# Kernel tuning notes

Measured on AMD Instinct MI355X. Metric: run time of the kernel, lower is better.

The kernel has to match this reference:

```python
import jax, jax.numpy as jnp
import numpy as np

N_ENTITIES = 100000
N_EDGES = 1250000
N_RELATIONS = 32
D = 64


def setup_inputs() -> dict:
    key = jax.random.key(0)
    k1, k2, k3, k4 = jax.random.split(key, 4)
    entity_emb = jax.random.normal(k1, (N_ENTITIES, D), dtype=jnp.float32)
    edge_index = jax.random.randint(k2, (2, N_EDGES), 0, N_ENTITIES, dtype=jnp.int64)
    edge_type = jax.random.randint(k3, (N_EDGES,), 0, N_RELATIONS, dtype=jnp.int64)
    weight = jax.random.normal(k4, (N_RELATIONS, D), dtype=jnp.float32)
    return {"entity_emb": entity_emb, "edge_index": edge_index,
            "edge_type": edge_type, "weight": weight}


def reference(entity_emb, edge_index, edge_type, weight):
    n_entities = entity_emb.shape[0]
    head, tail = edge_index[0], edge_index[1]
    # gather tail entity embeddings and relation embeddings, elementwise multiply
    neigh_relation_emb = entity_emb[tail] * weight[edge_type]  # [E, D]
    # scatter_mean by head index
    sums = jax.ops.segment_sum(neigh_relation_emb, head, num_segments=n_entities)
    counts = jax.ops.segment_sum(jnp.ones((head.shape[0],), dtype=entity_emb.dtype),
                                 head, num_segments=n_entities)
    entity_agg = sums / jnp.maximum(counts, 1.0)[:, None]  # empty segments -> 0
    return entity_agg
```

## Files before the change

### kernel.cpp

```cpp
#include <hip/hip_runtime.h>

#define D 64
#define BIN_SHIFT 7
#define BIN_SIZE 128
#define MAX_BINS 1024
#define BINCAP 2560
#define K1_THREADS 512
#define K1_EPT 10
#define K1_EPB (K1_THREADS * K1_EPT)
#define K2_THREADS 512
#define NREL 32


__device__ __forceinline__ float bf2f(unsigned short u) {
    union { unsigned i; float f; } x; x.i = ((unsigned)u) << 16; return x.f;
}

__global__ void cvt_kernel(const float* __restrict__ emb,
                           unsigned short* __restrict__ emb16,
                           int* __restrict__ binCount, int nbins, long n4) {
    long i = (long)blockIdx.x * blockDim.x + threadIdx.x;
    if (i < (long)nbins) binCount[i] = 0;
    if (i >= n4) return;
    float4 v = ((const float4*)emb)[i];
    ushort4 o;
    unsigned b;
    b = __float_as_uint(v.x); o.x = (unsigned short)((b + 0x7FFF + ((b >> 16) & 1)) >> 16);
    b = __float_as_uint(v.y); o.y = (unsigned short)((b + 0x7FFF + ((b >> 16) & 1)) >> 16);
    b = __float_as_uint(v.z); o.z = (unsigned short)((b + 0x7FFF + ((b >> 16) & 1)) >> 16);
    b = __float_as_uint(v.w); o.w = (unsigned short)((b + 0x7FFF + ((b >> 16) & 1)) >> 16);
    ((ushort4*)emb16)[i] = o;
}

__global__ void __launch_bounds__(K1_THREADS)
bin_sort_kernel(const int* __restrict__ head,
                const int* __restrict__ tail,
                const int* __restrict__ etype,
                int* __restrict__ binCount,
                unsigned* __restrict__ recs,
                int nbins, int n_edges) {
    __shared__ unsigned srec[K1_EPB];
    __shared__ int hist[MAX_BINS];
    __shared__ int base[MAX_BINS + 1];
    __shared__ int cur[MAX_BINS];
    __shared__ int gpos[MAX_BINS];
    __shared__ unsigned short binof[K1_EPB];
    __shared__ int wtot[8];
    __shared__ int wexcl[8];

    int tid = threadIdx.x;
    for (int b = tid; b < MAX_BINS; b += K1_THREADS) hist[b] = 0;
    __syncthreads();

    long blockBase = (long)blockIdx.x * K1_EPB;
    int nvalid = (int)(((long)n_edges - blockBase < (long)K1_EPB)
                       ? ((long)n_edges - blockBase) : (long)K1_EPB);

    unsigned rv[K1_EPT]; int bv[K1_EPT];
#pragma unroll
    for (int k = 0; k < K1_EPT; k++) {
        long e = blockBase + (long)k * K1_THREADS + tid;
        if (e < n_edges) {
            int h = head[e];
            bv[k] = h >> BIN_SHIFT;
            rv[k] = (unsigned)tail[e] | ((unsigned)etype[e] << 17)
                  | ((unsigned)(h & (BIN_SIZE - 1)) << 22);
            atomicAdd(&hist[bv[k]], 1);
        } else bv[k] = -1;
    }
    __syncthreads();

    int s0 = hist[2 * tid], s1 = hist[2 * tid + 1];
    int v = s0 + s1;
    int lane = tid & 63, wv = tid >> 6;
#pragma unroll
    for (int s = 1; s < 64; s <<= 1) {
        int x = __shfl_up(v, s);
        if (lane >= s) v += x;
    }
    if (lane == 63) wtot[wv] = v;
    __syncthreads();
    if (tid < 8) {
        int t = wtot[tid];
        int a = t;
#pragma unroll
        for (int s = 1; s < 8; s <<= 1) {
            int x = __shfl_up(a, s);
            if (tid >= s) a += x;
        }
        wexcl[tid] = a - t;
    }
    __syncthreads();
    int incl = v + wexcl[wv];
    int pairExcl = incl - (s0 + s1);
    base[2 * tid] = pairExcl;          cur[2 * tid] = pairExcl;
    base[2 * tid + 1] = pairExcl + s0; cur[2 * tid + 1] = pairExcl + s0;
    if (tid == K1_THREADS - 1) base[MAX_BINS] = incl;
    __syncthreads();

    for (int b = tid; b < nbins; b += K1_THREADS) {
        int c = hist[b];
        gpos[b] = (c > 0) ? atomicAdd(&binCount[b], c) : 0;
    }
    __syncthreads();

#pragma unroll
    for (int k = 0; k < K1_EPT; k++) {
        if (bv[k] >= 0) {
            int p = atomicAdd(&cur[bv[k]], 1);
            srec[p] = rv[k];
        }
    }
    __syncthreads();

    for (int b = tid; b < nbins; b += K1_THREADS) {
        int j0 = base[b], j1 = base[b + 1];
        for (int j = j0; j < j1; j++) binof[j] = (unsigned short)b;
    }
    __syncthreads();

    for (int i = tid; i < nvalid; i += K1_THREADS) {
        int b = binof[i];
        int off = gpos[b] + (i - base[b]);
        if (off < BINCAP)
            recs[(long)b * BINCAP + off] = srec[i];
    }
}

__global__ void __launch_bounds__(K2_THREADS, 2)
aggregate_bin_kernel(const unsigned short* __restrict__ emb16,
                     const float* __restrict__ weight,
                     const unsigned* __restrict__ recs,
                     const int* __restrict__ binCount,
                     float* __restrict__ out, int n_ent) {
    __shared__ unsigned raw[BINCAP];
    __shared__ unsigned sorted[BINCAP + 16];
    __shared__ float wlds[NREL * D];
    __shared__ float wz[D];
    __shared__ int hist[BIN_SIZE];
    __shared__ int off[BIN_SIZE];
    __shared__ int cur[BIN_SIZE];

    int tid = threadIdx.x;
    int b = blockIdx.x;
    int n = min(binCount[b], BINCAP);

    if (tid < 16) sorted[n + tid] = 0u;
    if (tid >= 448 && tid < 448 + D) wz[tid - 448] = 0.f;
    for (int i = tid; i < NREL * D; i += K2_THREADS) wlds[i] = weight[i];
    if (tid < BIN_SIZE) hist[tid] = 0;
    __syncthreads();

    const unsigned* gr = recs + (long)b * BINCAP;
    for (int i = tid; i < n; i += K2_THREADS) {
        unsigned q = gr[i];
        raw[i] = q;
        atomicAdd(&hist[(q >> 22) & 127], 1);
    }
    __syncthreads();

    int lane = tid & 63;
    int wave = tid >> 6;

    if (wave == 0) {
        int h0 = hist[lane];
        int h1 = hist[64 + lane];
        int s0 = h0, s1 = h1;
#pragma unroll
        for (int s = 1; s < 64; s <<= 1) {
            int t0 = __shfl_up(s0, s);
            int t1 = __shfl_up(s1, s);
            if (lane >= s) { s0 += t0; s1 += t1; }
        }
        int tot0 = __shfl(s0, 63);
        int e0 = s0 - h0;
        int e1 = tot0 + s1 - h1;
        off[lane] = e0;      cur[lane] = e0;
        off[64 + lane] = e1; cur[64 + lane] = e1;
    }
    __syncthreads();

    for (int i = tid; i < n; i += K2_THREADS) {
        unsigned q = raw[i];
        int p = atomicAdd(&cur[(q >> 22) & 127], 1);
        sorted[p] = q;
    }
    __syncthreads();

    int g = lane >> 4;
    int c4 = (lane & 15) << 2;
    int hbase = b << BIN_SHIFT;

    int oA, dA, oB, dB;
    unsigned qa0, qa1, qa2, qa3, qb0, qb1, qb2, qb3;
    ushort4 ua0, ua1, ua2, ua3, ub0, ub1, ub2, ub3;
    float4 wa0, wa1, wa2, wa3, wb0, wb1, wb2, wb3;

#define K2_PREF(J, o_, d_, q0, q1, q2, q3, u0, u1, u2, u3, w0, w1, w2, w3)    \
    do {                                                                       \
        int hh_ = wave + ((J) << 3);                                           \
        o_ = off[hh_]; d_ = hist[hh_];                                         \
        q0 = sorted[o_ + g];      q1 = sorted[o_ + 4 + g];                     \
        q2 = sorted[o_ + 8 + g];  q3 = sorted[o_ + 12 + g];                    \
        bool k0 = (g < d_), k1 = (4 + g < d_), k2 = (8 + g < d_),              \
             k3 = (12 + g < d_);                                               \
        q0 = k0 ? q0 : 0u;  q1 = k1 ? q1 : 0u;                                 \
        q2 = k2 ? q2 : 0u;  q3 = k3 ? q3 : 0u;                                 \
        u0 = *(const ushort4*)&emb16[((long)(q0 & 0x1FFFF) << 6) + c4];        \
        u1 = *(const ushort4*)&emb16[((long)(q1 & 0x1FFFF) << 6) + c4];        \
        u2 = *(const ushort4*)&emb16[((long)(q2 & 0x1FFFF) << 6) + c4];        \
        u3 = *(const ushort4*)&emb16[((long)(q3 & 0x1FFFF) << 6) + c4];        \
        w0 = *(const float4*)(k0 ? &wlds[(((q0 >> 17) & 31) << 6) + c4]        \
                                 : &wz[c4]);                                   \
        w1 = *(const float4*)(k1 ? &wlds[(((q1 >> 17) & 31) << 6) + c4]        \
                                 : &wz[c4]);                                   \
        w2 = *(const float4*)(k2 ? &wlds[(((q2 >> 17) & 31) << 6) + c4]        \
                                 : &wz[c4]);                                   \
        w3 = *(const float4*)(k3 ? &wlds[(((q3 >> 17) & 31) << 6) + c4]        \
                                 : &wz[c4]);                                   \
    } while (0)

#define K2_COMP(J, o_, d_, q0, q1, q2, q3, u0, u1, u2, u3, w0, w1, w2, w3)    \
    do {                                                                       \
        int hh_ = wave + ((J) << 3);                                           \
        float4 acc = make_float4(0.f, 0.f, 0.f, 0.f);                          \
        acc.x += bf2f(u0.x) * w0.x; acc.y += bf2f(u0.y) * w0.y;                \
        acc.z += bf2f(u0.z) * w0.z; acc.w += bf2f(u0.w) * w0.w;                \
        acc.x += bf2f(u1.x) * w1.x; acc.y += bf2f(u1.y) * w1.y;                \
        acc.z += bf2f(u1.z) * w1.z; acc.w += bf2f(u1.w) * w1.w;                \
        acc.x += bf2f(u2.x) * w2.x; acc.y += bf2f(u2.y) * w2.y;                \
        acc.z += bf2f(u2.z) * w2.z; acc.w += bf2f(u2.w) * w2.w;                \
        acc.x += bf2f(u3.x) * w3.x; acc.y += bf2f(u3.y) * w3.y;                \
        acc.z += bf2f(u3.z) * w3.z; acc.w += bf2f(u3.w) * w3.w;                \
        for (int i_ = 16; i_ < d_; i_ += 16) {          \
            int e0_ = i_ + g, e1_ = i_ + 4 + g, e2_ = i_ + 8 + g,              \
                e3_ = i_ + 12 + g;                                             \
            unsigned t0 = sorted[o_ + e0_]; unsigned t1 = sorted[o_ + e1_];    \
            unsigned t2 = sorted[o_ + e2_]; unsigned t3 = sorted[o_ + e3_];    \
            bool c0 = (e0_ < d_), c1 = (e1_ < d_), c2 = (e2_ < d_),            \
                 c3 = (e3_ < d_);                                              \
            t0 = c0 ? t0 : 0u;  t1 = c1 ? t1 : 0u;                             \
            t2 = c2 ? t2 : 0u;  t3 = c3 ? t3 : 0u;                             \
            ushort4 v0 = *(const ushort4*)&emb16[((long)(t0 & 0x1FFFF) << 6) + c4]; \
            ushort4 v1 = *(const ushort4*)&emb16[((long)(t1 & 0x1FFFF) << 6) + c4]; \
            ushort4 v2 = *(const ushort4*)&emb16[((long)(t2 & 0x1FFFF) << 6) + c4]; \
            ushort4 v3 = *(const ushort4*)&emb16[((long)(t3 & 0x1FFFF) << 6) + c4]; \
            float4 x0 = *(const float4*)(c0 ? &wlds[(((t0 >> 17) & 31) << 6) + c4] \
                                            : &wz[c4]);                        \
            float4 x1 = *(const float4*)(c1 ? &wlds[(((t1 >> 17) & 31) << 6) + c4] \
                                            : &wz[c4]);                        \
            float4 x2 = *(const float4*)(c2 ? &wlds[(((t2 >> 17) & 31) << 6) + c4] \
                                            : &wz[c4]);                        \
            float4 x3 = *(const float4*)(c3 ? &wlds[(((t3 >> 17) & 31) << 6) + c4] \
                                            : &wz[c4]);                        \
            acc.x += bf2f(v0.x) * x0.x; acc.y += bf2f(v0.y) * x0.y;            \
            acc.z += bf2f(v0.z) * x0.z; acc.w += bf2f(v0.w) * x0.w;            \
            acc.x += bf2f(v1.x) * x1.x; acc.y += bf2f(v1.y) * x1.y;            \
            acc.z += bf2f(v1.z) * x1.z; acc.w += bf2f(v1.w) * x1.w;            \
            acc.x += bf2f(v2.x) * x2.x; acc.y += bf2f(v2.y) * x2.y;            \
            acc.z += bf2f(v2.z) * x2.z; acc.w += bf2f(v2.w) * x2.w;            \
            acc.x += bf2f(v3.x) * x3.x; acc.y += bf2f(v3.y) * x3.y;            \
            acc.z += bf2f(v3.z) * x3.z; acc.w += bf2f(v3.w) * x3.w;            \
        }                                                                      \
        acc.x += __shfl_xor(acc.x, 16); acc.y += __shfl_xor(acc.y, 16);        \
        acc.z += __shfl_xor(acc.z, 16); acc.w += __shfl_xor(acc.w, 16);        \
        acc.x += __shfl_xor(acc.x, 32); acc.y += __shfl_xor(acc.y, 32);        \
        acc.z += __shfl_xor(acc.z, 32); acc.w += __shfl_xor(acc.w, 32);        \
        if (g == 0 && hbase + hh_ < n_ent) {                                   \
            float inv = 1.f / fmaxf((float)d_, 1.f);                           \
            *(float4*)&out[((long)(hbase + hh_) << 6) + c4] =                  \
                make_float4(acc.x * inv, acc.y * inv, acc.z * inv, acc.w * inv);\
        }                                                                      \
    } while (0)

    K2_PREF(0, oA, dA, qa0, qa1, qa2, qa3, ua0, ua1, ua2, ua3, wa0, wa1, wa2, wa3);
#pragma unroll 1
    for (int j = 0; j < 16; j += 2) {
        K2_PREF(j + 1, oB, dB, qb0, qb1, qb2, qb3, ub0, ub1, ub2, ub3,
                wb0, wb1, wb2, wb3);
        K2_COMP(j, oA, dA, qa0, qa1, qa2, qa3, ua0, ua1, ua2, ua3,
                wa0, wa1, wa2, wa3);
        int jn = (j + 2 < 16) ? (j + 2) : 15;
        K2_PREF(jn, oA, dA, qa0, qa1, qa2, qa3, ua0, ua1, ua2, ua3,
                wa0, wa1, wa2, wa3);
        K2_COMP(j + 1, oB, dB, qb0, qb1, qb2, qb3, ub0, ub1, ub2, ub3,
                wb0, wb1, wb2, wb3);
    }
#undef K2_PREF
#undef K2_COMP
}

__global__ void fb_scatter(const float* __restrict__ emb, const int* __restrict__ head,
                           const int* __restrict__ tail, const int* __restrict__ etype,
                           const float* __restrict__ weight, float* __restrict__ out,
                           float* __restrict__ cnt, int n_edges) {
    int gtid = blockIdx.x * blockDim.x + threadIdx.x;
    int e = gtid >> 6, lane = threadIdx.x & 63;
    if (e >= n_edges) return;
    int h = head[e], t = tail[e], r = etype[e];
    atomicAdd(&out[(long)h * D + lane], emb[(long)t * D + lane] * weight[r * D + lane]);
    if (lane == 0) atomicAdd(&cnt[h], 1.0f);
}
__global__ void fb_divide(float* __restrict__ out, const float* __restrict__ cnt, int n) {
    int i = blockIdx.x * blockDim.x + threadIdx.x;
    if (i < n) out[i] = out[i] / fmaxf(cnt[i >> 6], 1.0f);
}


extern "C" void kernel_launch(void* const* d_in, const int* in_sizes, int n_in,
                              void* d_out, int out_size, void* d_ws, size_t ws_size,
                              hipStream_t stream) {
    const float* emb    = (const float*)d_in[0];
    const int*   eidx   = (const int*)  d_in[1];
    const int*   etype  = (const int*)  d_in[2];
    const float* weight = (const float*)d_in[3];
    float* out = (float*)d_out;

    int n_edges = in_sizes[2];
    int n_ent   = out_size / D;
    const int* head = eidx;
    const int* tail = eidx + n_edges;

    int nbins = (n_ent + BIN_SIZE - 1) >> BIN_SHIFT;
    size_t recs_bytes = sizeof(int) * ((size_t)nbins * BINCAP);
    size_t cnt_bytes  = sizeof(int) * (size_t)nbins;
    size_t emb16_off  = (cnt_bytes + recs_bytes + 15) & ~((size_t)15);
    size_t need = emb16_off + (size_t)n_ent * D * sizeof(unsigned short);
    long mean_load = (n_ent > 0) ? ((long)n_edges * BIN_SIZE / n_ent) : 0;
    bool ok = (n_ent <= 131072) && (nbins <= MAX_BINS) && (ws_size >= need) &&
              (mean_load + 700 <= BINCAP);

    if (ok) {
        int* binCount  = (int*)d_ws;
        unsigned* recs = (unsigned*)(binCount + nbins);
        unsigned short* emb16 = (unsigned short*)((char*)d_ws + emb16_off);

        long n4 = (long)n_ent * D / 4;
        cvt_kernel<<<(int)((n4 + 255) / 256), 256, 0, stream>>>(
            emb, emb16, binCount, nbins, n4);

        int nblocks = (n_edges + K1_EPB - 1) / K1_EPB;
        bin_sort_kernel<<<nblocks, K1_THREADS, 0, stream>>>(
            head, tail, etype, binCount, recs, nbins, n_edges);

        aggregate_bin_kernel<<<nbins, K2_THREADS, 0, stream>>>(
            emb16, weight, recs, binCount, out, n_ent);
    } else {
        float* cnt = (float*)d_ws;
        hipMemsetAsync(out, 0, (size_t)out_size * sizeof(float), stream);
        hipMemsetAsync(cnt, 0, (size_t)n_ent * sizeof(float), stream);
        long tt = (long)n_edges * 64;
        fb_scatter<<<(int)((tt + 255) / 256), 256, 0, stream>>>(
            emb, head, tail, etype, weight, out, cnt, n_edges);
        fb_divide<<<(out_size + 255) / 256, 256, 0, stream>>>(out, cnt, out_size);
    }
}
```

Measured before the change: 147.2 us.

## Fuse bf16 conversion into bin-sort launch and widen sort blocks to 1024 threads

Merges the embedding fp32-to-bf16 conversion kernel into the binning sort kernel as extra blocks of the same launch, so conversion and edge binning run concurrently instead of back to back. The sort blocks move to 1024 threads with 5 edges per thread, so each thread owns one histogram bin in the scan. binCount zeroing moves to a hipMemsetAsync. This removes one kernel boundary at the cost of an extra memset and larger blocks that may hurt occupancy given the large shared memory per block.

Measured after the change: 146.1 us. Within noise of the previous version (-0.8%).

```diff
diff --git a/kernel.cpp b/kernel.cpp
--- a/kernel.cpp
+++ b/kernel.cpp
@@ -5,8 +5,8 @@
 #define BIN_SIZE 128
 #define MAX_BINS 1024
 #define BINCAP 2560
-#define K1_THREADS 512
-#define K1_EPT 10
+#define K1_THREADS 1024
+#define K1_EPT 5
 #define K1_EPB (K1_THREADS * K1_EPT)
 #define K2_THREADS 512
 #define NREL 32
@@ -16,40 +16,41 @@
     union { unsigned i; float f; } x; x.i = ((unsigned)u) << 16; return x.f;
 }
 
-__global__ void cvt_kernel(const float* __restrict__ emb,
-                           unsigned short* __restrict__ emb16,
-                           int* __restrict__ binCount, int nbins, long n4) {
-    long i = (long)blockIdx.x * blockDim.x + threadIdx.x;
-    if (i < (long)nbins) binCount[i] = 0;
-    if (i >= n4) return;
-    float4 v = ((const float4*)emb)[i];
-    ushort4 o;
-    unsigned b;
-    b = __float_as_uint(v.x); o.x = (unsigned short)((b + 0x7FFF + ((b >> 16) & 1)) >> 16);
-    b = __float_as_uint(v.y); o.y = (unsigned short)((b + 0x7FFF + ((b >> 16) & 1)) >> 16);
-    b = __float_as_uint(v.z); o.z = (unsigned short)((b + 0x7FFF + ((b >> 16) & 1)) >> 16);
-    b = __float_as_uint(v.w); o.w = (unsigned short)((b + 0x7FFF + ((b >> 16) & 1)) >> 16);
-    ((ushort4*)emb16)[i] = o;
-}
-
 __global__ void __launch_bounds__(K1_THREADS)
-bin_sort_kernel(const int* __restrict__ head,
-                const int* __restrict__ tail,
-                const int* __restrict__ etype,
-                int* __restrict__ binCount,
-                unsigned* __restrict__ recs,
-                int nbins, int n_edges) {
+prep_kernel(const float* __restrict__ emb,
+            unsigned short* __restrict__ emb16,
+            const int* __restrict__ head,
+            const int* __restrict__ tail,
+            const int* __restrict__ etype,
+            int* __restrict__ binCount,
+            unsigned* __restrict__ recs,
+            int nbins, int n_edges, long n4, int nsort) {
     __shared__ unsigned srec[K1_EPB];
     __shared__ int hist[MAX_BINS];
     __shared__ int base[MAX_BINS + 1];
     __shared__ int cur[MAX_BINS];
     __shared__ int gpos[MAX_BINS];
     __shared__ unsigned short binof[K1_EPB];
-    __shared__ int wtot[8];
-    __shared__ int wexcl[8];
+    __shared__ int wtot[16];
+    __shared__ int wexcl[16];
 
     int tid = threadIdx.x;
-    for (int b = tid; b < MAX_BINS; b += K1_THREADS) hist[b] = 0;
+
+    if (blockIdx.x >= nsort) {
+        long i = (long)(blockIdx.x - nsort) * K1_THREADS + tid;
+        if (i >= n4) return;
+        float4 v = ((const float4*)emb)[i];
+        ushort4 o;
+        unsigned b;
+        b = __float_as_uint(v.x); o.x = (unsigned short)((b + 0x7FFF + ((b >> 16) & 1)) >> 16);
+        b = __float_as_uint(v.y); o.y = (unsigned short)((b + 0x7FFF + ((b >> 16) & 1)) >> 16);
+        b = __float_as_uint(v.z); o.z = (unsigned short)((b + 0x7FFF + ((b >> 16) & 1)) >> 16);
+        b = __float_as_uint(v.w); o.w = (unsigned short)((b + 0x7FFF + ((b >> 16) & 1)) >> 16);
+        ((ushort4*)emb16)[i] = o;
+        return;
+    }
+
+    hist[tid] = 0;
     __syncthreads();
 
     long blockBase = (long)blockIdx.x * K1_EPB;
@@ -70,9 +71,9 @@
     }
     __syncthreads();
 
-    int s0 = hist[2 * tid], s1 = hist[2 * tid + 1];
-    int v = s0 + s1;
     int lane = tid & 63, wv = tid >> 6;
+    int h0 = hist[tid];
+    int v = h0;
 #pragma unroll
     for (int s = 1; s < 64; s <<= 1) {
         int x = __shfl_up(v, s);
@@ -80,27 +81,25 @@
     }
     if (lane == 63) wtot[wv] = v;
     __syncthreads();
-    if (tid < 8) {
-        int t = wtot[tid];
+    if (wv == 0 && lane < 16) {
+        int t = wtot[lane];
         int a = t;
 #pragma unroll
-        for (int s = 1; s < 8; s <<= 1) {
+        for (int s = 1; s < 16; s <<= 1) {
             int x = __shfl_up(a, s);
-            if (tid >= s) a += x;
+            if (lane >= s) a += x;
         }
-        wexcl[tid] = a - t;
+        wexcl[lane] = a - t;
     }
     __syncthreads();
     int incl = v + wexcl[wv];
-    int pairExcl = incl - (s0 + s1);
-    base[2 * tid] = pairExcl;          cur[2 * tid] = pairExcl;
-    base[2 * tid + 1] = pairExcl + s0; cur[2 * tid + 1] = pairExcl + s0;
+    base[tid] = incl - h0;  cur[tid] = incl - h0;
     if (tid == K1_THREADS - 1) base[MAX_BINS] = incl;
     __syncthreads();
 
-    for (int b = tid; b < nbins; b += K1_THREADS) {
-        int c = hist[b];
-        gpos[b] = (c > 0) ? atomicAdd(&binCount[b], c) : 0;
+    if (tid < nbins) {
+        int c = hist[tid];
+        gpos[tid] = (c > 0) ? atomicAdd(&binCount[tid], c) : 0;
     }
     __syncthreads();
 
@@ -113,9 +112,9 @@
     }
     __syncthreads();
 
-    for (int b = tid; b < nbins; b += K1_THREADS) {
-        int j0 = base[b], j1 = base[b + 1];
-        for (int j = j0; j < j1; j++) binof[j] = (unsigned short)b;
+    if (tid < nbins) {
+        int j0 = base[tid], j1 = base[tid + 1];
+        for (int j = j0; j < j1; j++) binof[j] = (unsigned short)tid;
     }
     __syncthreads();
 
@@ -336,12 +335,13 @@
         unsigned short* emb16 = (unsigned short*)((char*)d_ws + emb16_off);
 
         long n4 = (long)n_ent * D / 4;
-        cvt_kernel<<<(int)((n4 + 255) / 256), 256, 0, stream>>>(
-            emb, emb16, binCount, nbins, n4);
-
-        int nblocks = (n_edges + K1_EPB - 1) / K1_EPB;
-        bin_sort_kernel<<<nblocks, K1_THREADS, 0, stream>>>(
-            head, tail, etype, binCount, recs, nbins, n_edges);
+        int nsort = (n_edges + K1_EPB - 1) / K1_EPB;
+        int ncvt  = (int)((n4 + K1_THREADS - 1) / K1_THREADS);
+
+        hipMemsetAsync(binCount, 0, (size_t)nbins * sizeof(int), stream);
+        prep_kernel<<<nsort + ncvt, K1_THREADS, 0, stream>>>(
+            emb, emb16, head, tail, etype, binCount, recs,
+            nbins, n_edges, n4, nsort);
 
         aggregate_bin_kernel<<<nbins, K2_THREADS, 0, stream>>>(
             emb16, weight, recs, binCount, out, n_ent);
```
